# Performance work log

Measured on AMD Instinct MI355X. Metric: run time of the kernel, lower is better.

The kernel has to match this reference:

```python
import jax, jax.numpy as jnp
import numpy as np

# Conv hyperparams (from init_kwargs)
STRIDE = (1, 1)
PADDING = (1, 1)
DILATION = (1, 1)

AQMIN, AQMAX = 0.0, 15.0   # uint4 activation range
WQMIN, WQMAX = -8.0, 7.0   # int4 weight range


def setup_inputs() -> dict:
    key = jax.random.key(0)
    k1, k2 = jax.random.split(key)
    # Activations in [0, 16) so uint4 quantization is non-trivial
    x = jax.random.uniform(k1, (32, 64, 112, 112), dtype=jnp.float32) * 16.0
    # Weights spread over int4 range
    w = jax.random.normal(k2, (128, 64, 3, 3), dtype=jnp.float32) * 4.0
    return {"x": x, "w": w}


def reference(x, w):
    # Quantize: activations -> uint4 [0,15], weights -> int4 [-8,7]
    q_in = jnp.clip(jnp.round(x), AQMIN, AQMAX)
    q_w = jnp.clip(jnp.round(w), WQMIN, WQMAX)
    # im2col unfold + matmul in the original == standard convolution.
    # Integer-valued fp32 math is exact here (|acc| << 2^24).
    out = jax.lax.conv_general_dilated(
        q_in, q_w,
        window_strides=STRIDE,
        padding=[(PADDING[0], PADDING[0]), (PADDING[1], PADDING[1])],
        rhs_dilation=DILATION,
        dimension_numbers=("NCHW", "OIHW", "NCHW"),
    )
    return out.astype(jnp.float32)  # [32, 128, 112, 112]
```

## Files before the change

### kernel.cpp

```cpp
#include <hip/hip_runtime.h>


#define CIN  64
#define HH   112
#define WW   112
#define HW   (HH * WW)
#define COUT 128
#define HP   114
#define WP   114
#define KTOT 576

#define XQ_BYTES (32 * HP * WP * 64)
#define NWBLK 288
#define NXBLK (32 * 57)
#define NCONV 1792

#define SLAB_BYTES (4 * WP * 64)
#define SLAB_U16   (SLAB_BYTES / 16)

typedef __attribute__((ext_vector_type(4))) int int32x4;

__global__ __launch_bounds__(256) void k_prep(const float* __restrict__ x,
                                              const float* __restrict__ w,
                                              char* __restrict__ xq,
                                              char* __restrict__ wq) {
    const int bid = blockIdx.x, tid = threadIdx.x;
    if (bid < NWBLK) {
        int idx = bid * 256 + tid;
        int ks  = idx / 8192;
        int r2  = idx % 8192;
        int ct  = r2 / 1024;
        int r3  = r2 % 1024;
        int ln  = r3 / 16;
        int j   = r3 % 16;
        int o   = ct * 16 + (ln & 15);
        int c   = (ln >> 4) * 16 + j;
        int kh  = ks / 3, kw = ks % 3;
        float q = fminf(fmaxf(rintf(w[((o * CIN + c) * 3 + kh) * 3 + kw]), -8.0f), 7.0f);
        wq[idx] = (char)(int)q;
        return;
    }
    const int rid = bid - NWBLK;
    const int n  = rid / 57;
    const int hp = (rid % 57) * 2 + (tid >> 7);
    const int wp = tid & 127;
    if (wp >= WP) return;
    char* dst = xq + (((size_t)n * HP + hp) * WP + wp) * 64;
    int32x4* d4 = (int32x4*)dst;
    if (hp == 0 || hp == HP - 1 || wp == 0 || wp == WP - 1) {
#pragma unroll
        for (int i = 0; i < 4; ++i) d4[i] = (int32x4)(0);
        return;
    }
    const int h = hp - 1, ww = wp - 1;
    const float* px = x + (((size_t)n * CIN) * HH + h) * WW + ww;
    unsigned int buf[16];
#pragma unroll
    for (int cw = 0; cw < 16; ++cw) {
        unsigned int word = 0;
#pragma unroll
        for (int j = 0; j < 4; ++j) {
            float v = px[(size_t)(cw * 4 + j) * HW];
            float q = fminf(fmaxf(rintf(v), 0.0f), 15.0f);
            word |= ((unsigned int)(int)q) << (8 * j);
        }
        buf[cw] = word;
    }
#pragma unroll
    for (int i = 0; i < 4; ++i) {
        int32x4 v;
        v.x = (int)buf[i * 4 + 0];
        v.y = (int)buf[i * 4 + 1];
        v.z = (int)buf[i * 4 + 2];
        v.w = (int)buf[i * 4 + 3];
        d4[i] = v;
    }
}

__global__ __launch_bounds__(512, 4) void k_conv(const char* __restrict__ xq,
                                                 const char* __restrict__ wq,
                                                 float* __restrict__ out) {
    __shared__ char slab[SLAB_BYTES];

    const int tid = threadIdx.x;
    const int nid = (blockIdx.x & 7) * (NCONV / 8) + (blockIdx.x >> 3);
    const int n   = nid / 56;
    const int h0  = (nid % 56) * 2;

    const char* src = xq + (size_t)n * (HP * WP * 64) + (size_t)h0 * (WP * 64);
#pragma unroll
    for (int k = 0; k < 4; ++k) {
        const int u = tid + k * 512;
        if (u < SLAB_U16)
            *(int32x4*)(&slab[u * 16]) = *(const int32x4*)(src + u * 16);
    }
    __syncthreads();

    const int wave = tid >> 6;
    const int lane = tid & 63;
    const int l15  = lane & 15;
    const int lk   = lane >> 4;
    const int rw   = wave >> 2;
    const int Q    = wave & 3;

    const char* wbase = wq + (Q * 2) * 1024 + lane * 16;

    int32x4 acc[7][2];
#pragma unroll
    for (int i = 0; i < 7; ++i) {
        acc[i][0] = (int32x4)(0);
        acc[i][1] = (int32x4)(0);
    }

    int32x4 b0[2], b1[2], b2[2];
    b0[0] = *(const int32x4*)(wbase);
    b0[1] = *(const int32x4*)(wbase + 1024);
    b1[0] = *(const int32x4*)(wbase + 8192);
    b1[1] = *(const int32x4*)(wbase + 8192 + 1024);

#pragma unroll
    for (int ks = 0; ks < 9; ++ks) {
        {
            const int ksn = (ks + 2 <= 8) ? ks + 2 : 8;
            b2[0] = *(const int32x4*)(wbase + ksn * 8192);
            b2[1] = *(const int32x4*)(wbase + ksn * 8192 + 1024);
        }
        const int kh = ks / 3, kw = ks % 3;
        const char* arow = &slab[(((rw + kh) * WP) + l15 + kw) * 64 + lk * 16];
        int32x4 af[7];
#pragma unroll
        for (int wt = 0; wt < 7; ++wt)
            af[wt] = *(const int32x4*)(arow + wt * 1024);
#pragma unroll
        for (int tO = 0; tO < 2; ++tO)
#pragma unroll
            for (int wt = 0; wt < 7; ++wt)
                acc[wt][tO] = __builtin_amdgcn_mfma_i32_16x16x64_i8(af[wt], b0[tO], acc[wt][tO], 0, 0, 0);
        b0[0] = b1[0]; b0[1] = b1[1];
        b1[0] = b2[0]; b1[1] = b2[1];
    }

    const int hgl = h0 + rw;
#pragma unroll
    for (int wt = 0; wt < 7; ++wt) {
#pragma unroll
        for (int tO = 0; tO < 2; ++tO) {
            const int co = Q * 32 + tO * 16 + l15;
            float4 v;
            v.x = (float)acc[wt][tO][0];
            v.y = (float)acc[wt][tO][1];
            v.z = (float)acc[wt][tO][2];
            v.w = (float)acc[wt][tO][3];
            *(float4*)(&out[(((size_t)n * COUT + co) * HH + hgl) * WW + wt * 16 + lk * 4]) = v;
        }
    }
}

extern "C" void kernel_launch(void* const* d_in, const int* in_sizes, int n_in,
                              void* d_out, int out_size, void* d_ws, size_t ws_size,
                              hipStream_t stream) {
    const float* x = (const float*)d_in[0];
    const float* w = (const float*)d_in[1];
    float* out = (float*)d_out;

    char* xq = (char*)d_ws;
    char* wq = xq + XQ_BYTES;

    hipLaunchKernelGGL(k_prep, dim3(NWBLK + NXBLK), dim3(256), 0, stream, x, w, xq, wq);
    hipLaunchKernelGGL(k_conv, dim3(NCONV), dim3(512), 0, stream, xq, wq, out);
}
```

Baseline: 87.19 us.

## Process four output rows per block with async global-to-LDS slab loads

Each conv block now computes four output rows, split into two phases of two, instead of two. The input slab grows to six padded rows, so halo reuse improves. Loads use global_load_lds direct-to-LDS copies, and the last two slab rows are fetched while the first phase computes. The block count halves and LDS per block grows, which may cut occupancy and tail parallelism.

New measurement: 112.1 us. +28.6%, slower.

```diff
diff --git a/kernel.cpp b/kernel.cpp
--- a/kernel.cpp
+++ b/kernel.cpp
@@ -13,12 +13,20 @@
 #define XQ_BYTES (32 * HP * WP * 64)
 #define NWBLK 288
 #define NXBLK (32 * 57)
-#define NCONV 1792
-
-#define SLAB_BYTES (4 * WP * 64)
-#define SLAB_U16   (SLAB_BYTES / 16)
+#define NCONV 896
+
+#define ROWB (WP * 64)
+#define SLAB_BYTES (6 * ROWB)
+#define INIT_B (4 * ROWB)
+#define MID_B  (2 * ROWB)
 
 typedef __attribute__((ext_vector_type(4))) int int32x4;
+
+__device__ __forceinline__ void gld_lds16(const char* g, char* l) {
+    __builtin_amdgcn_global_load_lds(
+        (const __attribute__((address_space(1))) void*)g,
+        (__attribute__((address_space(3))) void*)l, 16, 0, 0);
+}
 
 __global__ __launch_bounds__(256) void k_prep(const float* __restrict__ x,
                                               const float* __restrict__ w,
@@ -84,75 +92,127 @@
 
     const int tid = threadIdx.x;
     const int nid = (blockIdx.x & 7) * (NCONV / 8) + (blockIdx.x >> 3);
-    const int n   = nid / 56;
-    const int h0  = (nid % 56) * 2;
-
-    const char* src = xq + (size_t)n * (HP * WP * 64) + (size_t)h0 * (WP * 64);
-#pragma unroll
-    for (int k = 0; k < 4; ++k) {
-        const int u = tid + k * 512;
-        if (u < SLAB_U16)
-            *(int32x4*)(&slab[u * 16]) = *(const int32x4*)(src + u * 16);
-    }
-    __syncthreads();
+    const int n   = nid / 28;
+    const int h0  = (nid % 28) * 4;
 
     const int wave = tid >> 6;
     const int lane = tid & 63;
-    const int l15  = lane & 15;
-    const int lk   = lane >> 4;
-    const int rw   = wave >> 2;
-    const int Q    = wave & 3;
+
+    const char* src = xq + (size_t)n * (HP * ROWB) + (size_t)h0 * ROWB;
+
+#pragma unroll
+    for (int k = 0; k < 4; ++k) {
+        const int ch  = wave + k * 8;
+        const int off = ch * 1024 + lane * 16;
+        if (off < INIT_B)
+            gld_lds16(src + off, slab + ch * 1024);
+    }
+    __syncthreads();
+
+#pragma unroll
+    for (int k = 0; k < 2; ++k) {
+        const int ch  = wave + k * 8;
+        const int off = ch * 1024 + lane * 16;
+        if (off < MID_B)
+            gld_lds16(src + INIT_B + off, slab + INIT_B + ch * 1024);
+    }
+
+    const int l15 = lane & 15;
+    const int lk  = lane >> 4;
+    const int rw  = wave >> 2;
+    const int Q   = wave & 3;
 
     const char* wbase = wq + (Q * 2) * 1024 + lane * 16;
 
-    int32x4 acc[7][2];
-#pragma unroll
-    for (int i = 0; i < 7; ++i) {
-        acc[i][0] = (int32x4)(0);
-        acc[i][1] = (int32x4)(0);
-    }
-
-    int32x4 b0[2], b1[2], b2[2];
-    b0[0] = *(const int32x4*)(wbase);
-    b0[1] = *(const int32x4*)(wbase + 1024);
-    b1[0] = *(const int32x4*)(wbase + 8192);
-    b1[1] = *(const int32x4*)(wbase + 8192 + 1024);
-
-#pragma unroll
-    for (int ks = 0; ks < 9; ++ks) {
-        {
+    int32x4 accA[7][2], accB[7][2];
+
+    {
+#pragma unroll
+        for (int i = 0; i < 7; ++i) { accA[i][0] = (int32x4)(0); accA[i][1] = (int32x4)(0); }
+        int32x4 b0[2], b1[2], b2[2];
+        b0[0] = *(const int32x4*)(wbase);
+        b0[1] = *(const int32x4*)(wbase + 1024);
+        b1[0] = *(const int32x4*)(wbase + 8192);
+        b1[1] = *(const int32x4*)(wbase + 8192 + 1024);
+#pragma unroll
+        for (int ks = 0; ks < 9; ++ks) {
             const int ksn = (ks + 2 <= 8) ? ks + 2 : 8;
             b2[0] = *(const int32x4*)(wbase + ksn * 8192);
             b2[1] = *(const int32x4*)(wbase + ksn * 8192 + 1024);
+            const int kh = ks / 3, kw = ks % 3;
+            const char* arow = &slab[(((rw + kh) * WP) + l15 + kw) * 64 + lk * 16];
+            int32x4 af[7];
+#pragma unroll
+            for (int wt = 0; wt < 7; ++wt)
+                af[wt] = *(const int32x4*)(arow + wt * 1024);
+#pragma unroll
+            for (int tO = 0; tO < 2; ++tO)
+#pragma unroll
+                for (int wt = 0; wt < 7; ++wt)
+                    accA[wt][tO] = __builtin_amdgcn_mfma_i32_16x16x64_i8(af[wt], b0[tO], accA[wt][tO], 0, 0, 0);
+            b0[0] = b1[0]; b0[1] = b1[1];
+            b1[0] = b2[0]; b1[1] = b2[1];
         }
-        const int kh = ks / 3, kw = ks % 3;
-        const char* arow = &slab[(((rw + kh) * WP) + l15 + kw) * 64 + lk * 16];
-        int32x4 af[7];
+    }
+
+    __syncthreads();
+
+    {
+        const int hgl = h0 + rw;
 #pragma unroll
         for (int wt = 0; wt < 7; ++wt)
-            af[wt] = *(const int32x4*)(arow + wt * 1024);
-#pragma unroll
-        for (int tO = 0; tO < 2; ++tO)
+#pragma unroll
+            for (int tO = 0; tO < 2; ++tO) {
+                const int co = Q * 32 + tO * 16 + l15;
+                float4 v;
+                v.x = (float)accA[wt][tO][0];
+                v.y = (float)accA[wt][tO][1];
+                v.z = (float)accA[wt][tO][2];
+                v.w = (float)accA[wt][tO][3];
+                *(float4*)(&out[(((size_t)n * COUT + co) * HH + hgl) * WW + wt * 16 + lk * 4]) = v;
+            }
+    }
+
+    {
+#pragma unroll
+        for (int i = 0; i < 7; ++i) { accB[i][0] = (int32x4)(0); accB[i][1] = (int32x4)(0); }
+        int32x4 b0[2], b1[2], b2[2];
+        b0[0] = *(const int32x4*)(wbase);
+        b0[1] = *(const int32x4*)(wbase + 1024);
+        b1[0] = *(const int32x4*)(wbase + 8192);
+        b1[1] = *(const int32x4*)(wbase + 8192 + 1024);
+#pragma unroll
+        for (int ks = 0; ks < 9; ++ks) {
+            const int ksn = (ks + 2 <= 8) ? ks + 2 : 8;
+            b2[0] = *(const int32x4*)(wbase + ksn * 8192);
+            b2[1] = *(const int32x4*)(wbase + ksn * 8192 + 1024);
+            const int kh = ks / 3, kw = ks % 3;
+            const char* arow = &slab[(((2 + rw + kh) * WP) + l15 + kw) * 64 + lk * 16];
+            int32x4 af[7];
 #pragma unroll
             for (int wt = 0; wt < 7; ++wt)
-                acc[wt][tO] = __builtin_amdgcn_mfma_i32_16x16x64_i8(af[wt], b0[tO], acc[wt][tO], 0, 0, 0);
-        b0[0] = b1[0]; b0[1] = b1[1];
-        b1[0] = b2[0]; b1[1] = b2[1];
-    }
-
-    const int hgl = h0 + rw;
-#pragma unroll
-    for (int wt = 0; wt < 7; ++wt) {
-#pragma unroll
-        for (int tO = 0; tO < 2; ++tO) {
-            const int co = Q * 32 + tO * 16 + l15;
-            float4 v;
-            v.x = (float)acc[wt][tO][0];
-            v.y = (float)acc[wt][tO][1];
-            v.z = (float)acc[wt][tO][2];
-            v.w = (float)acc[wt][tO][3];
-            *(float4*)(&out[(((size_t)n * COUT + co) * HH + hgl) * WW + wt * 16 + lk * 4]) = v;
+                af[wt] = *(const int32x4*)(arow + wt * 1024);
+#pragma unroll
+            for (int tO = 0; tO < 2; ++tO)
+#pragma unroll
+                for (int wt = 0; wt < 7; ++wt)
+                    accB[wt][tO] = __builtin_amdgcn_mfma_i32_16x16x64_i8(af[wt], b0[tO], accB[wt][tO], 0, 0, 0);
+            b0[0] = b1[0]; b0[1] = b1[1];
+            b1[0] = b2[0]; b1[1] = b2[1];
         }
+        const int hgl = h0 + 2 + rw;
+#pragma unroll
+        for (int wt = 0; wt < 7; ++wt)
+#pragma unroll
+            for (int tO = 0; tO < 2; ++tO) {
+                const int co = Q * 32 + tO * 16 + l15;
+                float4 v;
+                v.x = (float)accB[wt][tO][0];
+                v.y = (float)accB[wt][tO][1];
+                v.z = (float)accB[wt][tO][2];
+                v.w = (float)accB[wt][tO][3];
+                *(float4*)(&out[(((size_t)n * COUT + co) * HH + hgl) * WW + wt * 16 + lk * 4]) = v;
+            }
     }
 }
 
```
